# Kernel tuning notes

Measured on AMD Instinct MI355X. Metric: run time of the kernel, lower is better.

Reference implementation:

```python
import jax, jax.numpy as jnp
import numpy as np

EPS = 1e-20
ROUTING = 3
NUM_CAPS = 10
CAP_LEN = 16


def _squash_dim1(s):
    # Original torch Squash takes norm over dim=1; for s of shape [B,1,N,C]
    # that dim has size 1, so the norm degenerates to elementwise |s|.
    n = jnp.abs(s)
    return (n * n) / (1.0 + n * n) / (n + EPS) * s


def setup_inputs() -> dict:
    key = jax.random.key(0)
    k1, k2 = jax.random.split(key)
    B, h, w, Nin, Din = 32, 16, 16, 32, 8
    J = h * w * Nin
    x = jax.random.normal(k1, (B, h, w, Nin, Din), dtype=jnp.float32)
    # xavier-uniform-ish init for weight [J, Din, NUM_CAPS*CAP_LEN]
    fan_in, fan_out = Din, NUM_CAPS * CAP_LEN
    limit = float(np.sqrt(6.0 / (fan_in + fan_out)))
    weight = jax.random.uniform(k2, (J, Din, NUM_CAPS * CAP_LEN), dtype=jnp.float32,
                                minval=-limit, maxval=limit)
    biases = jnp.zeros((NUM_CAPS, CAP_LEN), dtype=jnp.float32)
    return {"x": x, "weight": weight, "biases": biases}


def reference(x, weight, biases):
    B, h, w, Nin, Din = x.shape
    J = h * w * Nin
    xf = x.reshape(B, J, Din)
    # pose projection: u[b,j,k] = sum_i x[b,j,i] * W[j,i,k]
    u = jnp.einsum('bji,jik->bjk', xf, weight)
    u = u.reshape(B, J, NUM_CAPS, CAP_LEN)
    b = jnp.zeros((B, J, NUM_CAPS, 1), dtype=u.dtype)
    v = None
    for r in range(ROUTING):
        c = jax.nn.softmax(b, axis=2)                      # [B,J,N,1]
        s = jnp.sum(u * c, axis=1, keepdims=True)          # [B,1,N,C]
        s = s + biases                                     # broadcast [N,C]
        v = _squash_dim1(s)                                # [B,1,N,C]
        if r < ROUTING - 1:
            b = b + jnp.sum(u * v, axis=-1, keepdims=True)  # agreement
    return v[:, 0]                                         # [B,N,C]
```

## Files before the change

### kernel.cpp

```cpp
#include <hip/hip_runtime.h>

#define NB 32
#define NJ 8192
#define NC 10
#define CL 16
#define KK 160
#define JT 16
#define NTHR 640
#define BCH 4
#define NPART (NJ / JT)
#define REP 8
#define EPSQ 1e-20f

template<int CTRL>
__device__ __forceinline__ float dpp_add(float v) {
    int s = __builtin_amdgcn_update_dpp(0, __float_as_int(v), CTRL, 0xF, 0xF, true);
    return v + __int_as_float(s);
}
__device__ __forceinline__ float red16(float v) {
    v = dpp_add<0xB1>(v);
    v = dpp_add<0x4E>(v);
    v = dpp_add<0x141>(v);
    v = dpp_add<0x140>(v);
    return v;
}

template<int R, bool ATOM>
__global__ __launch_bounds__(NTHR, 5)
void rout_kernel(const float* __restrict__ x, const float* __restrict__ W,
                 const float* __restrict__ vsum, float* __restrict__ sdst) {
    __shared__ float xs[NB][JT][10];
    __shared__ float vsl[NB][KK];
    __shared__ float bl[BCH][JT][12];
    __shared__ float cl[BCH][JT][12];

    const int t   = threadIdx.x;
    const int jj  = t & 15;
    const int k4  = t >> 4;
    const int nB  = k4 >> 2;
    const int c4  = k4 & 3;
    const int j0  = blockIdx.x * JT;

    float4 w[8];
    {
        const float* wp = W + ((size_t)(j0 + jj) * 8) * KK + (k4 << 2);
        #pragma unroll
        for (int i = 0; i < 8; ++i)
            w[i] = *(const float4*)(wp + i * KK);
    }
    for (int e4 = t; e4 < NB * JT * 2; e4 += NTHR) {
        const int b = e4 >> 5, rem = e4 & 31, jx = rem >> 1, hf = rem & 1;
        const float4 v = *(const float4*)(x + ((size_t)b * NJ + j0 + jx) * 8 + hf * 4);
        float* d = &xs[b][jx][hf * 4];
        d[0] = v.x; d[1] = v.y; d[2] = v.z; d[3] = v.w;
    }
    if (R > 0) {
        for (int f4 = t; f4 < NB * 40; f4 += NTHR) {
            const int b = f4 / 40, rem = f4 % 40;
            *(float4*)&vsl[b][rem * 4] = *(const float4*)(vsum + (size_t)b * KK + rem * 4);
        }
    }
    __syncthreads();

    for (int b0 = 0; b0 < NB; b0 += BCH) {
        float4 u[BCH];
        #pragma unroll
        for (int bc = 0; bc < BCH; ++bc) {
            const int b = b0 + bc;
            float4 acc = {0.f, 0.f, 0.f, 0.f};
            #pragma unroll
            for (int seg = 0; seg < 4; ++seg) {
                const float2 xv = *(const float2*)&xs[b][jj][seg * 2];
                const float4 wa = w[seg * 2], wb = w[seg * 2 + 1];
                acc.x = fmaf(wa.x, xv.x, acc.x); acc.y = fmaf(wa.y, xv.x, acc.y);
                acc.z = fmaf(wa.z, xv.x, acc.z); acc.w = fmaf(wa.w, xv.x, acc.w);
                acc.x = fmaf(wb.x, xv.y, acc.x); acc.y = fmaf(wb.y, xv.y, acc.y);
                acc.z = fmaf(wb.z, xv.y, acc.z); acc.w = fmaf(wb.w, xv.y, acc.w);
            }
            u[bc] = acc;
        }

        if (R > 0) {
            #pragma unroll
            for (int bc = 0; bc < BCH; ++bc) {
                const int b = b0 + bc;
                const float4 vv = *(const float4*)&vsl[b][k4 * 4];
                float bd = u[bc].x * vv.x + u[bc].y * vv.y
                         + u[bc].z * vv.z + u[bc].w * vv.w;
                bd += __shfl_xor(bd, 16);
                bd += __shfl_xor(bd, 32);
                if (c4 == 0) bl[bc][jj][nB] = bd;
            }
            __syncthreads();
            {
                const int bcC = t / 160, rem = t % 160;
                const int jjC = rem & 15, nn = rem >> 4;
                float m = -1e30f;
                #pragma unroll
                for (int q = 0; q < NC; ++q) m = fmaxf(m, bl[bcC][jjC][q]);
                float sum = 0.f;
                #pragma unroll
                for (int q = 0; q < NC; ++q) sum += __expf(bl[bcC][jjC][q] - m);
                cl[bcC][jjC][nn] = __expf(bl[bcC][jjC][nn] - m) / sum;
            }
            __syncthreads();
        }

        #pragma unroll
        for (int bc = 0; bc < BCH; ++bc) {
            const int b = b0 + bc;
            const float c = (R == 0) ? 0.1f : cl[bc][jj][nB];
            const float sx = red16(u[bc].x * c);
            const float sy = red16(u[bc].y * c);
            const float sz = red16(u[bc].z * c);
            const float sw = red16(u[bc].w * c);
            if (jj == 0) {
                if (ATOM) {
                    float* sp = sdst + ((size_t)(blockIdx.x & (REP - 1)) * NB + b) * KK + (k4 << 2);
                    atomicAdd(sp + 0, sx); atomicAdd(sp + 1, sy);
                    atomicAdd(sp + 2, sz); atomicAdd(sp + 3, sw);
                } else {
                    float4 q; q.x = sx; q.y = sy; q.z = sz; q.w = sw;
                    *(float4*)(sdst + ((size_t)blockIdx.x * NB + b) * KK + (k4 << 2)) = q;
                }
            }
        }
    }
}

template<int MODE>
__global__ __launch_bounds__(1024)
void reduce_squash(const float* __restrict__ part, const float* __restrict__ biases,
                   float* __restrict__ vsum, float* __restrict__ out) {
    __shared__ float4 red[16][64];
    const int t   = threadIdx.x;
    const int col = t & 63;
    const int pc  = t >> 6;
    const int g   = blockIdx.x * 64 + col;
    const float4* p4 = (const float4*)part;

    float4 acc = {0.f, 0.f, 0.f, 0.f};
    #pragma unroll 4
    for (int p = pc * 32; p < pc * 32 + 32; ++p) {
        const float4 v = p4[(size_t)p * (NB * KK / 4) + g];
        acc.x += v.x; acc.y += v.y; acc.z += v.z; acc.w += v.w;
    }
    red[pc][col] = acc;
    __syncthreads();
    if (pc == 0) {
        #pragma unroll
        for (int q = 1; q < 16; ++q) {
            const float4 v = red[q][col];
            acc.x += v.x; acc.y += v.y; acc.z += v.z; acc.w += v.w;
        }
        const int k4 = g % 40;
        const float4 bb = *(const float4*)(biases + k4 * 4);
        float4 v;
        {
            const float s0 = acc.x + bb.x, n0 = fabsf(s0);
            v.x = (n0 * n0) / (1.f + n0 * n0) / (n0 + EPSQ) * s0;
            const float s1 = acc.y + bb.y, n1 = fabsf(s1);
            v.y = (n1 * n1) / (1.f + n1 * n1) / (n1 + EPSQ) * s1;
            const float s2 = acc.z + bb.z, n2 = fabsf(s2);
            v.z = (n2 * n2) / (1.f + n2 * n2) / (n2 + EPSQ) * s2;
            const float s3 = acc.w + bb.w, n3 = fabsf(s3);
            v.w = (n3 * n3) / (1.f + n3 * n3) / (n3 + EPSQ) * s3;
        }
        if (MODE == 2) {
            ((float4*)out)[g] = v;
        } else if (MODE == 1) {
            float4 o = ((float4*)vsum)[g];
            o.x += v.x; o.y += v.y; o.z += v.z; o.w += v.w;
            ((float4*)vsum)[g] = o;
        } else {
            ((float4*)vsum)[g] = v;
        }
    }
}

template<int MODE>
__global__ __launch_bounds__(256)
void squash_kernel(float* __restrict__ s_part, const float* __restrict__ biases,
                   float* __restrict__ vsum, float* __restrict__ out) {
    const int t = blockIdx.x * blockDim.x + threadIdx.x;
    if (t >= NB * KK) return;
    float s = 0.f;
    #pragma unroll
    for (int r = 0; r < REP; ++r) {
        s += s_part[(size_t)r * (NB * KK) + t];
        s_part[(size_t)r * (NB * KK) + t] = 0.f;
    }
    s += biases[t % KK];
    const float n = fabsf(s);
    const float v = (n * n) / (1.f + n * n) / (n + EPSQ) * s;
    if (MODE == 2)      out[t]   = v;
    else if (MODE == 1) vsum[t] += v;
    else                vsum[t]  = v;
}

extern "C" void kernel_launch(void* const* d_in, const int* in_sizes, int n_in,
                              void* d_out, int out_size, void* d_ws, size_t ws_size,
                              hipStream_t stream) {
    const float* x      = (const float*)d_in[0];
    const float* W      = (const float*)d_in[1];
    const float* biases = (const float*)d_in[2];
    float* out = (float*)d_out;

    const size_t store_need = ((size_t)NPART * NB * KK + NB * KK) * sizeof(float);
    const dim3 grid(NJ / JT);

    if (ws_size >= store_need) {
        float* part = (float*)d_ws;
        float* vsum = part + (size_t)NPART * NB * KK;

        rout_kernel<0, false><<<grid, NTHR, 0, stream>>>(x, W, nullptr, part);
        reduce_squash<0><<<20, 1024, 0, stream>>>(part, biases, vsum, out);

        rout_kernel<1, false><<<grid, NTHR, 0, stream>>>(x, W, vsum, part);
        reduce_squash<1><<<20, 1024, 0, stream>>>(part, biases, vsum, out);

        rout_kernel<2, false><<<grid, NTHR, 0, stream>>>(x, W, vsum, part);
        reduce_squash<2><<<20, 1024, 0, stream>>>(part, biases, vsum, out);
    } else {
        float* s_part = (float*)d_ws;
        float* vsum   = s_part + (size_t)REP * NB * KK;

        hipMemsetAsync(s_part, 0, (size_t)REP * NB * KK * sizeof(float), stream);

        rout_kernel<0, true><<<grid, NTHR, 0, stream>>>(x, W, nullptr, s_part);
        squash_kernel<0><<<20, 256, 0, stream>>>(s_part, biases, vsum, out);

        rout_kernel<1, true><<<grid, NTHR, 0, stream>>>(x, W, vsum, s_part);
        squash_kernel<1><<<20, 256, 0, stream>>>(s_part, biases, vsum, out);

        rout_kernel<2, true><<<grid, NTHR, 0, stream>>>(x, W, vsum, s_part);
        squash_kernel<2><<<20, 256, 0, stream>>>(s_part, biases, vsum, out);
    }
}
```

Measured before the change: 126.0 us.

## Split batch across a second grid dimension and drop the atomic fallback path

The routing kernel now launches a 2D grid with the batch split into two halves of 16, so each block stages only its half of x in shared memory. The vsum shared staging is removed and vsum is read directly from global memory. The atomic-accumulation fallback path and its squash kernel are deleted. This doubles block count for better occupancy and smaller LDS, at the cost of loading each W tile twice (once per batch half) and unconditionally assuming a large enough workspace.

Result: slower. 147.9 us (+17.4%).

```diff
diff --git a/kernel.cpp b/kernel.cpp
--- a/kernel.cpp
+++ b/kernel.cpp
@@ -7,9 +7,9 @@
 #define KK 160
 #define JT 16
 #define NTHR 640
+#define BB 16
 #define BCH 4
 #define NPART (NJ / JT)
-#define REP 8
 #define EPSQ 1e-20f
 
 template<int CTRL>
@@ -25,12 +25,11 @@
     return v;
 }
 
-template<int R, bool ATOM>
+template<int R>
 __global__ __launch_bounds__(NTHR, 5)
 void rout_kernel(const float* __restrict__ x, const float* __restrict__ W,
-                 const float* __restrict__ vsum, float* __restrict__ sdst) {
-    __shared__ float xs[NB][JT][10];
-    __shared__ float vsl[NB][KK];
+                 const float* __restrict__ vsum, float* __restrict__ part) {
+    __shared__ float xs[BB][JT][10];
     __shared__ float bl[BCH][JT][12];
     __shared__ float cl[BCH][JT][12];
 
@@ -40,6 +39,7 @@
     const int nB  = k4 >> 2;
     const int c4  = k4 & 3;
     const int j0  = blockIdx.x * JT;
+    const int bof = blockIdx.y * BB;
 
     float4 w[8];
     {
@@ -48,29 +48,22 @@
         for (int i = 0; i < 8; ++i)
             w[i] = *(const float4*)(wp + i * KK);
     }
-    for (int e4 = t; e4 < NB * JT * 2; e4 += NTHR) {
-        const int b = e4 >> 5, rem = e4 & 31, jx = rem >> 1, hf = rem & 1;
-        const float4 v = *(const float4*)(x + ((size_t)b * NJ + j0 + jx) * 8 + hf * 4);
-        float* d = &xs[b][jx][hf * 4];
+    for (int e4 = t; e4 < BB * JT * 2; e4 += NTHR) {
+        const int bb = e4 >> 5, rem = e4 & 31, jx = rem >> 1, hf = rem & 1;
+        const float4 v = *(const float4*)(x + ((size_t)(bof + bb) * NJ + j0 + jx) * 8 + hf * 4);
+        float* d = &xs[bb][jx][hf * 4];
         d[0] = v.x; d[1] = v.y; d[2] = v.z; d[3] = v.w;
-    }
-    if (R > 0) {
-        for (int f4 = t; f4 < NB * 40; f4 += NTHR) {
-            const int b = f4 / 40, rem = f4 % 40;
-            *(float4*)&vsl[b][rem * 4] = *(const float4*)(vsum + (size_t)b * KK + rem * 4);
-        }
     }
     __syncthreads();
 
-    for (int b0 = 0; b0 < NB; b0 += BCH) {
+    for (int b0 = 0; b0 < BB; b0 += BCH) {
         float4 u[BCH];
         #pragma unroll
         for (int bc = 0; bc < BCH; ++bc) {
-            const int b = b0 + bc;
             float4 acc = {0.f, 0.f, 0.f, 0.f};
             #pragma unroll
             for (int seg = 0; seg < 4; ++seg) {
-                const float2 xv = *(const float2*)&xs[b][jj][seg * 2];
+                const float2 xv = *(const float2*)&xs[b0 + bc][jj][seg * 2];
                 const float4 wa = w[seg * 2], wb = w[seg * 2 + 1];
                 acc.x = fmaf(wa.x, xv.x, acc.x); acc.y = fmaf(wa.y, xv.x, acc.y);
                 acc.z = fmaf(wa.z, xv.x, acc.z); acc.w = fmaf(wa.w, xv.x, acc.w);
@@ -83,8 +76,8 @@
         if (R > 0) {
             #pragma unroll
             for (int bc = 0; bc < BCH; ++bc) {
-                const int b = b0 + bc;
-                const float4 vv = *(const float4*)&vsl[b][k4 * 4];
+                const int b = bof + b0 + bc;
+                const float4 vv = *(const float4*)(vsum + (size_t)b * KK + (k4 << 2));
                 float bd = u[bc].x * vv.x + u[bc].y * vv.y
                          + u[bc].z * vv.z + u[bc].w * vv.w;
                 bd += __shfl_xor(bd, 16);
@@ -108,21 +101,15 @@
 
         #pragma unroll
         for (int bc = 0; bc < BCH; ++bc) {
-            const int b = b0 + bc;
+            const int b = bof + b0 + bc;
             const float c = (R == 0) ? 0.1f : cl[bc][jj][nB];
             const float sx = red16(u[bc].x * c);
             const float sy = red16(u[bc].y * c);
             const float sz = red16(u[bc].z * c);
             const float sw = red16(u[bc].w * c);
             if (jj == 0) {
-                if (ATOM) {
-                    float* sp = sdst + ((size_t)(blockIdx.x & (REP - 1)) * NB + b) * KK + (k4 << 2);
-                    atomicAdd(sp + 0, sx); atomicAdd(sp + 1, sy);
-                    atomicAdd(sp + 2, sz); atomicAdd(sp + 3, sw);
-                } else {
-                    float4 q; q.x = sx; q.y = sy; q.z = sz; q.w = sw;
-                    *(float4*)(sdst + ((size_t)blockIdx.x * NB + b) * KK + (k4 << 2)) = q;
-                }
+                float4 q; q.x = sx; q.y = sy; q.z = sz; q.w = sw;
+                *(float4*)(part + ((size_t)blockIdx.x * NB + b) * KK + (k4 << 2)) = q;
             }
         }
     }
@@ -178,62 +165,24 @@
     }
 }
 
-template<int MODE>
-__global__ __launch_bounds__(256)
-void squash_kernel(float* __restrict__ s_part, const float* __restrict__ biases,
-                   float* __restrict__ vsum, float* __restrict__ out) {
-    const int t = blockIdx.x * blockDim.x + threadIdx.x;
-    if (t >= NB * KK) return;
-    float s = 0.f;
-    #pragma unroll
-    for (int r = 0; r < REP; ++r) {
-        s += s_part[(size_t)r * (NB * KK) + t];
-        s_part[(size_t)r * (NB * KK) + t] = 0.f;
-    }
-    s += biases[t % KK];
-    const float n = fabsf(s);
-    const float v = (n * n) / (1.f + n * n) / (n + EPSQ) * s;
-    if (MODE == 2)      out[t]   = v;
-    else if (MODE == 1) vsum[t] += v;
-    else                vsum[t]  = v;
-}
-
 extern "C" void kernel_launch(void* const* d_in, const int* in_sizes, int n_in,
                               void* d_out, int out_size, void* d_ws, size_t ws_size,
                               hipStream_t stream) {
     const float* x      = (const float*)d_in[0];
     const float* W      = (const float*)d_in[1];
     const float* biases = (const float*)d_in[2];
-    float* out = (float*)d_out;
+    float* out  = (float*)d_out;
+    float* part = (float*)d_ws;
+    float* vsum = part + (size_t)NPART * NB * KK;
 
-    const size_t store_need = ((size_t)NPART * NB * KK + NB * KK) * sizeof(float);
-    const dim3 grid(NJ / JT);
+    const dim3 grid(NJ / JT, NB / BB);
 
-    if (ws_size >= store_need) {
-        float* part = (float*)d_ws;
-        float* vsum = part + (size_t)NPART * NB * KK;
+    rout_kernel<0><<<grid, NTHR, 0, stream>>>(x, W, nullptr, part);
+    reduce_squash<0><<<20, 1024, 0, stream>>>(part, biases, vsum, out);
 
-        rout_kernel<0, false><<<grid, NTHR, 0, stream>>>(x, W, nullptr, part);
-        reduce_squash<0><<<20, 1024, 0, stream>>>(part, biases, vsum, out);
+    rout_kernel<1><<<grid, NTHR, 0, stream>>>(x, W, vsum, part);
+    reduce_squash<1><<<20, 1024, 0, stream>>>(part, biases, vsum, out);
 
-        rout_kernel<1, false><<<grid, NTHR, 0, stream>>>(x, W, vsum, part);
-        reduce_squash<1><<<20, 1024, 0, stream>>>(part, biases, vsum, out);
-
-        rout_kernel<2, false><<<grid, NTHR, 0, stream>>>(x, W, vsum, part);
-        reduce_squash<2><<<20, 1024, 0, stream>>>(part, biases, vsum, out);
-    } else {
-        float* s_part = (float*)d_ws;
-        float* vsum   = s_part + (size_t)REP * NB * KK;
-
-        hipMemsetAsync(s_part, 0, (size_t)REP * NB * KK * sizeof(float), stream);
-
-        rout_kernel<0, true><<<grid, NTHR, 0, stream>>>(x, W, nullptr, s_part);
-        squash_kernel<0><<<20, 256, 0, stream>>>(s_part, biases, vsum, out);
-
-        rout_kernel<1, true><<<grid, NTHR, 0, stream>>>(x, W, vsum, s_part);
-        squash_kernel<1><<<20, 256, 0, stream>>>(s_part, biases, vsum, out);
-
-        rout_kernel<2, true><<<grid, NTHR, 0, stream>>>(x, W, vsum, s_part);
-        squash_kernel<2><<<20, 256, 0, stream>>>(s_part, biases, vsum, out);
-    }
+    rout_kernel<2><<<grid, NTHR, 0, stream>>>(x, W, vsum, part);
+    reduce_squash<2><<<20, 1024, 0, stream>>>(part, biases, vsum, out);
 }
```

## Pre-transpose weight into coalesced layout before routing kernels

Applied to the files above, without the earlier changes.

Adds a transpose kernel that rewrites W into a per-block, per-thread contiguous float4 layout in the workspace, so each routing pass loads weights with fully coalesced accesses. The atomic-based low-workspace fallback is dropped and the old store path becomes the fallback. This adds a full read and write of the 42MB weight each call in exchange for cleaner loads in three passes.

Result: slower. 139.5 us (+10.7%).

```diff
diff --git a/kernel.cpp b/kernel.cpp
--- a/kernel.cpp
+++ b/kernel.cpp
@@ -9,7 +9,6 @@
 #define NTHR 640
 #define BCH 4
 #define NPART (NJ / JT)
-#define REP 8
 #define EPSQ 1e-20f
 
 template<int CTRL>
@@ -25,10 +24,35 @@
     return v;
 }
 
-template<int R, bool ATOM>
+__global__ __launch_bounds__(NTHR)
+void transpose_w(const float* __restrict__ W, float* __restrict__ Wt) {
+    __shared__ float4 lds[16 * 165];
+    const int t  = threadIdx.x;
+    const int jx = blockIdx.x, ih = blockIdx.y;
+    const float4* W4 = (const float4*)W;
+    float4* Wt4 = (float4*)Wt;
+
+    {
+        const int jj = t / 40, col = t % 40;
+        #pragma unroll
+        for (int q = 0; q < 4; ++q)
+            lds[jj * 165 + q * 41 + col] =
+                W4[((size_t)(jx * 16 + jj)) * 320 + (ih * 4 + q) * 40 + col];
+    }
+    __syncthreads();
+    {
+        const int jj = t & 15, k4 = t >> 4;
+        #pragma unroll
+        for (int q = 0; q < 4; ++q)
+            Wt4[((size_t)jx * 8 + ih * 4 + q) * 640 + t] =
+                lds[jj * 165 + q * 41 + k4];
+    }
+}
+
+template<int R, bool TR>
 __global__ __launch_bounds__(NTHR, 5)
-void rout_kernel(const float* __restrict__ x, const float* __restrict__ W,
-                 const float* __restrict__ vsum, float* __restrict__ sdst) {
+void rout_kernel(const float* __restrict__ x, const float* __restrict__ Wp,
+                 const float* __restrict__ vsum, float* __restrict__ part) {
     __shared__ float xs[NB][JT][10];
     __shared__ float vsl[NB][KK];
     __shared__ float bl[BCH][JT][12];
@@ -42,8 +66,13 @@
     const int j0  = blockIdx.x * JT;
 
     float4 w[8];
-    {
-        const float* wp = W + ((size_t)(j0 + jj) * 8) * KK + (k4 << 2);
+    if (TR) {
+        const float4* wt = (const float4*)Wp + (size_t)blockIdx.x * 8 * 640 + t;
+        #pragma unroll
+        for (int i = 0; i < 8; ++i)
+            w[i] = wt[i * 640];
+    } else {
+        const float* wp = Wp + ((size_t)(j0 + jj) * 8) * KK + (k4 << 2);
         #pragma unroll
         for (int i = 0; i < 8; ++i)
             w[i] = *(const float4*)(wp + i * KK);
@@ -66,11 +95,10 @@
         float4 u[BCH];
         #pragma unroll
         for (int bc = 0; bc < BCH; ++bc) {
-            const int b = b0 + bc;
             float4 acc = {0.f, 0.f, 0.f, 0.f};
             #pragma unroll
             for (int seg = 0; seg < 4; ++seg) {
-                const float2 xv = *(const float2*)&xs[b][jj][seg * 2];
+                const float2 xv = *(const float2*)&xs[b0 + bc][jj][seg * 2];
                 const float4 wa = w[seg * 2], wb = w[seg * 2 + 1];
                 acc.x = fmaf(wa.x, xv.x, acc.x); acc.y = fmaf(wa.y, xv.x, acc.y);
                 acc.z = fmaf(wa.z, xv.x, acc.z); acc.w = fmaf(wa.w, xv.x, acc.w);
@@ -83,8 +111,7 @@
         if (R > 0) {
             #pragma unroll
             for (int bc = 0; bc < BCH; ++bc) {
-                const int b = b0 + bc;
-                const float4 vv = *(const float4*)&vsl[b][k4 * 4];
+                const float4 vv = *(const float4*)&vsl[b0 + bc][k4 * 4];
                 float bd = u[bc].x * vv.x + u[bc].y * vv.y
                          + u[bc].z * vv.z + u[bc].w * vv.w;
                 bd += __shfl_xor(bd, 16);
@@ -115,14 +142,8 @@
             const float sz = red16(u[bc].z * c);
             const float sw = red16(u[bc].w * c);
             if (jj == 0) {
-                if (ATOM) {
-                    float* sp = sdst + ((size_t)(blockIdx.x & (REP - 1)) * NB + b) * KK + (k4 << 2);
-                    atomicAdd(sp + 0, sx); atomicAdd(sp + 1, sy);
-                    atomicAdd(sp + 2, sz); atomicAdd(sp + 3, sw);
-                } else {
-                    float4 q; q.x = sx; q.y = sy; q.z = sz; q.w = sw;
-                    *(float4*)(sdst + ((size_t)blockIdx.x * NB + b) * KK + (k4 << 2)) = q;
-                }
+                float4 q; q.x = sx; q.y = sy; q.z = sz; q.w = sw;
+                *(float4*)(part + ((size_t)blockIdx.x * NB + b) * KK + (k4 << 2)) = q;
             }
         }
     }
@@ -178,26 +199,6 @@
     }
 }
 
-template<int MODE>
-__global__ __launch_bounds__(256)
-void squash_kernel(float* __restrict__ s_part, const float* __restrict__ biases,
-                   float* __restrict__ vsum, float* __restrict__ out) {
-    const int t = blockIdx.x * blockDim.x + threadIdx.x;
-    if (t >= NB * KK) return;
-    float s = 0.f;
-    #pragma unroll
-    for (int r = 0; r < REP; ++r) {
-        s += s_part[(size_t)r * (NB * KK) + t];
-        s_part[(size_t)r * (NB * KK) + t] = 0.f;
-    }
-    s += biases[t % KK];
-    const float n = fabsf(s);
-    const float v = (n * n) / (1.f + n * n) / (n + EPSQ) * s;
-    if (MODE == 2)      out[t]   = v;
-    else if (MODE == 1) vsum[t] += v;
-    else                vsum[t]  = v;
-}
-
 extern "C" void kernel_launch(void* const* d_in, const int* in_sizes, int n_in,
                               void* d_out, int out_size, void* d_ws, size_t ws_size,
                               hipStream_t stream) {
@@ -206,10 +207,26 @@
     const float* biases = (const float*)d_in[2];
     float* out = (float*)d_out;
 
-    const size_t store_need = ((size_t)NPART * NB * KK + NB * KK) * sizeof(float);
+    const size_t wt_f  = (size_t)NJ * 8 * KK;
+    const size_t need  = (wt_f + (size_t)NPART * NB * KK + NB * KK) * sizeof(float);
     const dim3 grid(NJ / JT);
 
-    if (ws_size >= store_need) {
+    if (ws_size >= need) {
+        float* Wt   = (float*)d_ws;
+        float* part = Wt + wt_f;
+        float* vsum = part + (size_t)NPART * NB * KK;
+
+        transpose_w<<<dim3(NJ / JT, 2), NTHR, 0, stream>>>(W, Wt);
+
+        rout_kernel<0, true><<<grid, NTHR, 0, stream>>>(x, Wt, nullptr, part);
+        reduce_squash<0><<<20, 1024, 0, stream>>>(part, biases, vsum, out);
+
+        rout_kernel<1, true><<<grid, NTHR, 0, stream>>>(x, Wt, vsum, part);
+        reduce_squash<1><<<20, 1024, 0, stream>>>(part, biases, vsum, out);
+
+        rout_kernel<2, true><<<grid, NTHR, 0, stream>>>(x, Wt, vsum, part);
+        reduce_squash<2><<<20, 1024, 0, stream>>>(part, biases, vsum, out);
+    } else {
         float* part = (float*)d_ws;
         float* vsum = part + (size_t)NPART * NB * KK;
 
@@ -221,19 +238,5 @@
 
         rout_kernel<2, false><<<grid, NTHR, 0, stream>>>(x, W, vsum, part);
         reduce_squash<2><<<20, 1024, 0, stream>>>(part, biases, vsum, out);
-    } else {
-        float* s_part = (float*)d_ws;
-        float* vsum   = s_part + (size_t)REP * NB * KK;
-
-        hipMemsetAsync(s_part, 0, (size_t)REP * NB * KK * sizeof(float), stream);
-
-        rout_kernel<0, true><<<grid, NTHR, 0, stream>>>(x, W, nullptr, s_part);
-        squash_kernel<0><<<20, 256, 0, stream>>>(s_part, biases, vsum, out);
-
-        rout_kernel<1, true><<<grid, NTHR, 0, stream>>>(x, W, vsum, s_part);
-        squash_kernel<1><<<20, 256, 0, stream>>>(s_part, biases, vsum, out);
-
-        rout_kernel<2, true><<<grid, NTHR, 0, stream>>>(x, W, vsum, s_part);
-        squash_kernel<2><<<20, 256, 0, stream>>>(s_part, biases, vsum, out);
-    }
-}
+    }
+}
```
